# Optimization experiments

Hardware: AMD Instinct MI355X
Metric: run time of the kernel (lower is better)

The kernel has to match this reference:

```python
import jax, jax.numpy as jnp
import numpy as np

N_NODES = 50000
N_EDGES = 1600000
IN_DIM = 128
HID = 64
N_GRAPHS = 256


def gcn_conv(x, row, col, W, b, n_nodes):
    """PyG GCNConv: symmetric gcn_norm with self-loops, linear-then-aggregate."""
    h = x @ W  # [N, out]
    loop = jnp.arange(n_nodes, dtype=row.dtype)
    r = jnp.concatenate([row, loop])  # sources (messages from x[r])
    c = jnp.concatenate([col, loop])  # targets (aggregate at c)
    ew = jnp.ones(r.shape[0], dtype=x.dtype)
    deg = jax.ops.segment_sum(ew, c, num_segments=n_nodes)
    dinv = jnp.where(deg > 0, jax.lax.rsqrt(deg), 0.0).astype(x.dtype)
    norm = dinv[r] * dinv[c]  # [E+N]
    out = jax.ops.segment_sum(norm[:, None] * h[r], c, num_segments=n_nodes)
    return out + b


def global_mean_pool(x, batch, n_graphs):
    sums = jax.ops.segment_sum(x, batch, num_segments=n_graphs)
    cnt = jax.ops.segment_sum(jnp.ones(x.shape[0], x.dtype), batch, num_segments=n_graphs)
    return sums / jnp.clip(cnt, 1.0)[:, None]


def setup_inputs() -> dict:
    key = jax.random.key(0)
    ks = jax.random.split(key, 12)
    x = jax.random.normal(ks[0], (N_NODES, IN_DIM), dtype=jnp.float32)
    edge_index = jax.random.randint(ks[1], (2, N_EDGES), 0, N_NODES, dtype=jnp.int64)
    batch = jnp.sort(jax.random.randint(ks[2], (N_NODES,), 0, N_GRAPHS, dtype=jnp.int64))
    def glorot(k, shp):
        lim = float(np.sqrt(6.0 / (shp[0] + shp[1])))
        return jax.random.uniform(k, shp, jnp.float32, -lim, lim)
    return {
        "x": x,
        "edge_index": edge_index,
        "batch": batch,
        "W1": glorot(ks[3], (IN_DIM, HID)), "b1": jnp.zeros((HID,), jnp.float32),
        "W2": glorot(ks[4], (HID, HID)), "b2": jnp.zeros((HID,), jnp.float32),
        "W3": glorot(ks[5], (HID, HID)), "b3": jnp.zeros((HID,), jnp.float32),
        "Wl1": glorot(ks[6], (HID, 16)), "bl1": jnp.zeros((16,), jnp.float32),
        "Wl2": glorot(ks[7], (16, 1)), "bl2": jnp.zeros((1,), jnp.float32),
    }


def reference(x, edge_index, batch, W1, b1, W2, b2, W3, b3, Wl1, bl1, Wl2, bl2):
    n = x.shape[0]
    row, col = edge_index[0], edge_index[1]
    h = jax.nn.relu(gcn_conv(x, row, col, W1, b1, n))
    h = jax.nn.relu(gcn_conv(h, row, col, W2, b2, n))
    h = jax.nn.relu(gcn_conv(h, row, col, W3, b3, n))
    g = global_mean_pool(h, batch, N_GRAPHS)  # [G, 64]
    out = (g @ Wl1 + bl1) @ Wl2 + bl2  # [G, 1]
    return out
```

## Files before the change

kernel.cpp:

```cpp
#include <hip/hip_runtime.h>

#define HID 64
#define B1 512
#define NBMAX 200
#define CAP 10368
#define ENTCAP 3200
#define CPT 21

typedef __attribute__((ext_vector_type(8))) short short8;
typedef __attribute__((ext_vector_type(4))) float float4v;
typedef float f32x2 __attribute__((ext_vector_type(2)));

__device__ __forceinline__ ushort f2bf(float f) {
  unsigned u = __float_as_uint(f);
  unsigned r = (u + 0x7fffu + ((u >> 16) & 1u)) >> 16;
  return (ushort)r;
}
__device__ __forceinline__ float bf2f(ushort v) {
  return __uint_as_float(((unsigned)v) << 16);
}

__device__ __forceinline__ void acc8(f32x2& a01, f32x2& a23, uint2 d) {
  f32x2 t0, t1;
  t0.x = __uint_as_float(d.x << 16);
  t0.y = __uint_as_float(d.x & 0xffff0000u);
  t1.x = __uint_as_float(d.y << 16);
  t1.y = __uint_as_float(d.y & 0xffff0000u);
  a01 += t0;
  a23 += t1;
}


__global__ __launch_bounds__(256) void bucket_hist(const int* __restrict__ col, int E, int epb,
                                                   int* __restrict__ blockcnt,
                                                   const float* __restrict__ W1,
                                                   const float* __restrict__ W2,
                                                   const float* __restrict__ W3,
                                                   ushort* __restrict__ Wt1h, ushort* __restrict__ Wt1l,
                                                   ushort* __restrict__ Wt2h, ushort* __restrict__ Wt2l,
                                                   ushort* __restrict__ Wt3h, ushort* __restrict__ Wt3l) {
  int b = blockIdx.x, t = threadIdx.x;
  int gt = b * 256 + t;
  if (gt < 128 * 64) {
    int k = gt >> 6, nn = gt & 63;
    float w = W1[gt];
    ushort h = f2bf(w);
    Wt1h[nn * 128 + k] = h;
    Wt1l[nn * 128 + k] = f2bf(w - bf2f(h));
  }
  if (gt < 64 * 64) {
    int k = gt >> 6, nn = gt & 63;
    float w2 = W2[gt], w3 = W3[gt];
    ushort h2 = f2bf(w2), h3 = f2bf(w3);
    Wt2h[nn * 64 + k] = h2;
    Wt2l[nn * 64 + k] = f2bf(w2 - bf2f(h2));
    Wt3h[nn * 64 + k] = h3;
    Wt3l[nn * 64 + k] = f2bf(w3 - bf2f(h3));
  }

  __shared__ int cnt[256];
  cnt[t] = 0;
  __syncthreads();
  int lo = b * epb, hi = min(lo + epb, E);
  int ecnt = hi - lo;
  if (ecnt > 0) {
    int ecnt4 = ecnt & ~3;
    for (int i = t * 4; i < ecnt4; i += 1024) {
      int4 c4 = *(const int4*)&col[lo + i];
      atomicAdd(&cnt[c4.x >> 8], 1);
      atomicAdd(&cnt[c4.y >> 8], 1);
      atomicAdd(&cnt[c4.z >> 8], 1);
      atomicAdd(&cnt[c4.w >> 8], 1);
    }
    for (int i = ecnt4 + t; i < ecnt; i += 256) atomicAdd(&cnt[col[lo + i] >> 8], 1);
  }
  __syncthreads();
  blockcnt[b * 256 + t] = cnt[t];
}

__global__ __launch_bounds__(512) void scan_blocks(int* __restrict__ blockcnt,
                                                   int* __restrict__ buckettot) {
  __shared__ int s[512];
  int k = blockIdx.x;
  int t = threadIdx.x;
  int v = blockcnt[t * 256 + k];
  s[t] = v;
  __syncthreads();
  for (int d = 1; d < 512; d <<= 1) {
    int u = (t >= d) ? s[t - d] : 0;
    __syncthreads();
    s[t] += u;
    __syncthreads();
  }
  blockcnt[t * 256 + k] = s[t] - v;
  if (t == 511) buckettot[k] = s[t];
}

__global__ __launch_bounds__(256) void scan_buckettot(const int* __restrict__ buckettot,
                                                      int* __restrict__ bucketbase,
                                                      int* __restrict__ csr_off, int n, int E,
                                                      int nb) {
  __shared__ int s[256];
  int t = threadIdx.x;
  int v = buckettot[t];
  s[t] = v;
  __syncthreads();
  for (int d = 1; d < 256; d <<= 1) {
    int u = (t >= d) ? s[t - d] : 0;
    __syncthreads();
    s[t] += u;
    __syncthreads();
  }
  bucketbase[t] = s[t] - v;
  if (t == 255) bucketbase[256] = s[255];
  if (t == 0) csr_off[n] = E;
}

__global__ __launch_bounds__(256) void bin_edges(const int* __restrict__ row,
                                                 const int* __restrict__ col, int E, int epb,
                                                 const int* __restrict__ blockcnt,
                                                 const int* __restrict__ bucketbase,
                                                 unsigned* __restrict__ binned) {
  __shared__ int cnt[256];
  __shared__ int ofs[256];
  __shared__ int gb[256];
  __shared__ int lcur[256];
  __shared__ unsigned ent[ENTCAP];
  __shared__ unsigned stage[ENTCAP];
  int b = blockIdx.x, t = threadIdx.x;
  int lo = b * epb, hi = min(lo + epb, E);
  int ecnt = hi - lo;

  cnt[t] = 0;
  __syncthreads();
  if (ecnt > 0) {
    int ecnt4 = ecnt & ~3;
    for (int i = t * 4; i < ecnt4; i += 1024) {
      int4 c4 = *(const int4*)&col[lo + i];
      int4 r4 = *(const int4*)&row[lo + i];
      uint4 e4;
      e4.x = ((unsigned)r4.x << 16) | (unsigned)c4.x;
      e4.y = ((unsigned)r4.y << 16) | (unsigned)c4.y;
      e4.z = ((unsigned)r4.z << 16) | (unsigned)c4.z;
      e4.w = ((unsigned)r4.w << 16) | (unsigned)c4.w;
      *(uint4*)&ent[i] = e4;
      atomicAdd(&cnt[c4.x >> 8], 1);
      atomicAdd(&cnt[c4.y >> 8], 1);
      atomicAdd(&cnt[c4.z >> 8], 1);
      atomicAdd(&cnt[c4.w >> 8], 1);
    }
    for (int i = ecnt4 + t; i < ecnt; i += 256) {
      int c = col[lo + i];
      int r = row[lo + i];
      ent[i] = ((unsigned)r << 16) | (unsigned)c;
      atomicAdd(&cnt[c >> 8], 1);
    }
  }
  __syncthreads();
  int v = cnt[t];
  ofs[t] = v;
  __syncthreads();
  for (int d = 1; d < 256; d <<= 1) {
    int u = (t >= d) ? ofs[t - d] : 0;
    __syncthreads();
    ofs[t] += u;
    __syncthreads();
  }
  int excl = ofs[t] - v;
  int g = bucketbase[t] + blockcnt[b * 256 + t];
  __syncthreads();
  ofs[t] = excl;
  gb[t] = g;
  lcur[t] = excl;
  __syncthreads();
  if (ecnt > 0) {
    for (int i = t; i < ecnt; i += 256) {
      unsigned en = ent[i];
      int p = atomicAdd(&lcur[(en >> 8) & 255], 1);
      stage[p] = en;
    }
  }
  __syncthreads();
  if (ecnt > 0) {
    for (int i = t; i < ecnt; i += 256) {
      unsigned en = stage[i];
      int bb = (en >> 8) & 255;
      binned[gb[bb] + (i - ofs[bb])] = en;
    }
  }
}

__global__ __launch_bounds__(512) void bucket_csr(const unsigned* __restrict__ binned,
                                                  const int* __restrict__ bucketbase,
                                                  int* __restrict__ csr_off,
                                                  int* __restrict__ csr_src,
                                                  float* __restrict__ dinv, int n) {
  __shared__ int lcnt[256];
  __shared__ int lofs[256];
  __shared__ int lsrc[CAP];
  int k = blockIdx.x, t = threadIdx.x;
  int base = bucketbase[k], end = bucketbase[k + 1];
  int s = end - base;
  unsigned ent[CPT];
  if (t < 256) lcnt[t] = 0;
  __syncthreads();
#pragma unroll
  for (int q = 0; q < CPT; ++q) {
    int i = q * 512 + t;
    if (i < s) {
      unsigned p = binned[base + i];
      ent[q] = p;
      atomicAdd(&lcnt[p & 255u], 1);
    }
  }
  __syncthreads();
  int v = 0;
  if (t < 256) {
    v = lcnt[t];
    lofs[t] = v;
  }
  __syncthreads();
  for (int d = 1; d < 256; d <<= 1) {
    int u = (t < 256 && t >= d) ? lofs[t - d] : 0;
    __syncthreads();
    if (t < 256) lofs[t] += u;
    __syncthreads();
  }
  if (t < 256) {
    int excl = lofs[t] - v;
    int node = (k << 8) + t;
    if (node < n) {
      csr_off[node] = base + excl;
      dinv[node] = rsqrtf((float)(v + 1));
    }
    lcnt[t] = excl;
  }
  __syncthreads();
#pragma unroll
  for (int q = 0; q < CPT; ++q) {
    int i = q * 512 + t;
    if (i < s) {
      unsigned p = ent[q];
      int pos = atomicAdd(&lcnt[p & 255u], 1);
      if (pos < CAP) lsrc[pos] = (int)(p >> 16);
    }
  }
  __syncthreads();
  for (int i = t; i < s; i += 512) csr_src[base + i] = (i < CAP) ? lsrc[i] : 0;
}


template <int K>
__global__ __launch_bounds__(256) void gemm_mfma(const float* __restrict__ A,
                                                 const ushort* __restrict__ Wh,
                                                 const ushort* __restrict__ Wl,
                                                 const float* __restrict__ dinv,
                                                 ushort* __restrict__ out, int n) {
  int wave = (blockIdx.x * 256 + threadIdx.x) >> 6;
  int lane = threadIdx.x & 63;
  int row0 = wave * 16;
  if (row0 >= n) return;
  int m = lane & 15;
  int quad = lane >> 4;
  int r = row0 + m;
  int rc = (r < n) ? r : (n - 1);

  float4v acc[4];
#pragma unroll
  for (int t = 0; t < 4; ++t) acc[t] = (float4v){0.f, 0.f, 0.f, 0.f};

#pragma unroll
  for (int k0 = 0; k0 < K; k0 += 32) {
    const float4* xp = (const float4*)&A[(size_t)rc * K + k0 + quad * 8];
    float4 a0 = xp[0];
    float4 a1 = xp[1];
    float av[8] = {a0.x, a0.y, a0.z, a0.w, a1.x, a1.y, a1.z, a1.w};
    short8 ah, al;
#pragma unroll
    for (int i = 0; i < 8; ++i) {
      ushort h = f2bf(av[i]);
      ah[i] = (short)h;
      al[i] = (short)f2bf(av[i] - bf2f(h));
    }
#pragma unroll
    for (int t = 0; t < 4; ++t) {
      size_t wof = (size_t)(t * 16 + m) * K + k0 + quad * 8;
      short8 bh = *(const short8*)&Wh[wof];
      short8 bl = *(const short8*)&Wl[wof];
      acc[t] = __builtin_amdgcn_mfma_f32_16x16x32_bf16(ah, bh, acc[t], 0, 0, 0);
      acc[t] = __builtin_amdgcn_mfma_f32_16x16x32_bf16(al, bh, acc[t], 0, 0, 0);
      acc[t] = __builtin_amdgcn_mfma_f32_16x16x32_bf16(ah, bl, acc[t], 0, 0, 0);
    }
  }

  float4 dv = ((const float4*)dinv)[(row0 >> 2) + quad];
  float dvi[4] = {dv.x, dv.y, dv.z, dv.w};
#pragma unroll
  for (int i = 0; i < 4; ++i) {
    int orow = row0 + quad * 4 + i;
    if (orow < n) {
#pragma unroll
      for (int t = 0; t < 4; ++t) {
        out[(size_t)orow * 64 + t * 16 + m] = f2bf(dvi[i] * acc[t][i]);
      }
    }
  }
}


__global__ __launch_bounds__(256) void agg_kernel(
    const ushort* __restrict__ hs, const int* __restrict__ csr_off,
    const int* __restrict__ csr_src, const float* __restrict__ dinv,
    const float* __restrict__ bias, float* __restrict__ out, int n) {
  int wid = (blockIdx.x * 256 + threadIdx.x) >> 6;
  int lane = threadIdx.x & 63;
  if (wid >= n) return;
  int qe = lane >> 4;
  int fq = lane & 15;
  const uint2* hs2 = (const uint2*)hs;

  f32x2 a01 = {0.f, 0.f}, a23 = {0.f, 0.f};
  if (qe == 0) {
    acc8(a01, a23, hs2[(size_t)wid * 16 + fq]);
  }

  int j = csr_off[wid];
  int e = csr_off[wid + 1];

  int pre = min(e, (j + 3) & ~3);
  if (j + qe < pre) {
    int s0 = csr_src[j + qe];
    acc8(a01, a23, hs2[(size_t)s0 * 16 + fq]);
  }
  int base = pre;

  for (; base + 16 <= e; base += 16) {
    int4 s = *(const int4*)&csr_src[base + qe * 4];
    uint2 v0 = hs2[(size_t)s.x * 16 + fq];
    uint2 v1 = hs2[(size_t)s.y * 16 + fq];
    uint2 v2 = hs2[(size_t)s.z * 16 + fq];
    uint2 v3 = hs2[(size_t)s.w * 16 + fq];
    acc8(a01, a23, v0);
    acc8(a01, a23, v1);
    acc8(a01, a23, v2);
    acc8(a01, a23, v3);
  }

  for (; base + 4 <= e; base += 4) {
    int s0 = csr_src[base + qe];
    acc8(a01, a23, hs2[(size_t)s0 * 16 + fq]);
  }
  if (base + qe < e) {
    int s0 = csr_src[base + qe];
    acc8(a01, a23, hs2[(size_t)s0 * 16 + fq]);
  }

  a01.x += __shfl_xor(a01.x, 16, 64);
  a01.y += __shfl_xor(a01.y, 16, 64);
  a23.x += __shfl_xor(a23.x, 16, 64);
  a23.y += __shfl_xor(a23.y, 16, 64);
  a01.x += __shfl_xor(a01.x, 32, 64);
  a01.y += __shfl_xor(a01.y, 32, 64);
  a23.x += __shfl_xor(a23.x, 32, 64);
  a23.y += __shfl_xor(a23.y, 32, 64);

  if (qe == 0) {
    float d = dinv[wid];
    float4 bi = ((const float4*)bias)[fq];
    float4 r;
    r.x = fmaxf(d * a01.x + bi.x, 0.f);
    r.y = fmaxf(d * a01.y + bi.y, 0.f);
    r.z = fmaxf(d * a23.x + bi.z, 0.f);
    r.w = fmaxf(d * a23.y + bi.w, 0.f);
    ((float4*)out)[(size_t)wid * 16 + fq] = r;
  }
}


__global__ __launch_bounds__(256) void pool_mlp_kernel(
    const float* __restrict__ a, const int* __restrict__ batch, int n,
    const float* __restrict__ Wl1, const float* __restrict__ bl1,
    const float* __restrict__ Wl2, const float* __restrict__ bl2,
    float* __restrict__ out) {
  int g = blockIdx.x;
  int t = threadIdx.x;
  int lane = t & 63;
  int w = t >> 6;

  int lo = 0, hi = n;
  while (lo < hi) {
    int m = (lo + hi) >> 1;
    if (batch[m] < g) lo = m + 1; else hi = m;
  }
  int start = lo;
  lo = start; hi = n;
  while (lo < hi) {
    int m = (lo + hi) >> 1;
    if (batch[m] < g + 1) lo = m + 1; else hi = m;
  }
  int end = lo;

  float s = 0.f;
  for (int i = start + w; i < end; i += 4) s += a[i * 64 + lane];

  __shared__ float ps[4][64];
  __shared__ float gv[64];
  __shared__ float hv[16];
  ps[w][lane] = s;
  __syncthreads();
  if (w == 0) {
    float tot = ps[0][lane] + ps[1][lane] + ps[2][lane] + ps[3][lane];
    gv[lane] = tot / (float)max(end - start, 1);
  }
  __syncthreads();
  if (t < 16) {
    float h = bl1[t];
    for (int k = 0; k < 64; ++k) h += gv[k] * Wl1[k * 16 + t];
    hv[t] = h;
  }
  __syncthreads();
  if (t == 0) {
    float o = bl2[0];
    for (int j2 = 0; j2 < 16; ++j2) o += hv[j2] * Wl2[j2];
    out[g] = o;
  }
}


extern "C" void kernel_launch(void* const* d_in, const int* in_sizes, int n_in,
                              void* d_out, int out_size, void* d_ws, size_t ws_size,
                              hipStream_t stream) {
  const float* x = (const float*)d_in[0];
  const int* ei = (const int*)d_in[1];
  const int* batch = (const int*)d_in[2];
  const float* W1 = (const float*)d_in[3];
  const float* b1 = (const float*)d_in[4];
  const float* W2 = (const float*)d_in[5];
  const float* b2 = (const float*)d_in[6];
  const float* W3 = (const float*)d_in[7];
  const float* b3 = (const float*)d_in[8];
  const float* Wl1 = (const float*)d_in[9];
  const float* bl1 = (const float*)d_in[10];
  const float* Wl2 = (const float*)d_in[11];
  const float* bl2 = (const float*)d_in[12];

  int n = in_sizes[0] / 128;
  int E = in_sizes[1] / 2;
  int G = out_size;
  int nb = (n + 255) >> 8;
  int epb = (((E + B1 - 1) / B1) + 15) & ~15;

  const int* row = ei;
  const int* col = ei + E;

  char* p = (char*)d_ws;
  int* blockcnt = (int*)p;    p += B1 * 256 * 4;
  int* buckettot = (int*)p;   p += 256 * 4;
  int* bucketbase = (int*)p;  p += 272 * 4;
  int* csr_off = (int*)p;     p += 50064 * 4;
  float* dinv = (float*)p;    p += 50016 * 4;
  ushort* Wt1h = (ushort*)p;  p += 128 * 64 * 2;
  ushort* Wt1l = (ushort*)p;  p += 128 * 64 * 2;
  ushort* Wt2h = (ushort*)p;  p += 64 * 64 * 2;
  ushort* Wt2l = (ushort*)p;  p += 64 * 64 * 2;
  ushort* Wt3h = (ushort*)p;  p += 64 * 64 * 2;
  ushort* Wt3l = (ushort*)p;  p += 64 * 64 * 2;
  int* csr_src = (int*)p;     p += (size_t)((E + 15) / 16 * 16) * 4;
  ushort* hs = (ushort*)p;    p += (size_t)n * 64 * 2;
  float* abuf = (float*)p;
  unsigned* binned = (unsigned*)hs;

  bucket_hist<<<B1, 256, 0, stream>>>(col, E, epb, blockcnt,
                                      W1, W2, W3, Wt1h, Wt1l, Wt2h, Wt2l, Wt3h, Wt3l);
  scan_blocks<<<256, 512, 0, stream>>>(blockcnt, buckettot);
  scan_buckettot<<<1, 256, 0, stream>>>(buckettot, bucketbase, csr_off, n, E, nb);
  bin_edges<<<B1, 256, 0, stream>>>(row, col, E, epb, blockcnt, bucketbase, binned);
  bucket_csr<<<nb, 512, 0, stream>>>(binned, bucketbase, csr_off, csr_src, dinv, n);

  int nwaves = (n + 15) / 16;
  int gblocks = (nwaves + 3) / 4;
  int ablocks = (n * 64 + 255) / 256;

  gemm_mfma<128><<<gblocks, 256, 0, stream>>>(x, Wt1h, Wt1l, dinv, hs, n);
  agg_kernel<<<ablocks, 256, 0, stream>>>(hs, csr_off, csr_src, dinv, b1, abuf, n);
  gemm_mfma<64><<<gblocks, 256, 0, stream>>>(abuf, Wt2h, Wt2l, dinv, hs, n);
  agg_kernel<<<ablocks, 256, 0, stream>>>(hs, csr_off, csr_src, dinv, b2, abuf, n);
  gemm_mfma<64><<<gblocks, 256, 0, stream>>>(abuf, Wt3h, Wt3l, dinv, hs, n);
  agg_kernel<<<ablocks, 256, 0, stream>>>(hs, csr_off, csr_src, dinv, b3, abuf, n);
  pool_mlp_kernel<<<G, 256, 0, stream>>>(abuf, batch, n, Wl1, bl1, Wl2, bl2, (float*)d_out);
}
```

Baseline: 306.9 us.

## Fuse CSR build stages into one cooperative kernel with grid syncs

```diff
diff --git a/kernel.cpp b/kernel.cpp
--- a/kernel.cpp
+++ b/kernel.cpp
@@ -1,4 +1,7 @@
 #include <hip/hip_runtime.h>
+#include <hip/hip_cooperative_groups.h>
+
+namespace cg = cooperative_groups;
 
 #define HID 64
 #define B1 512
@@ -31,16 +34,26 @@
 }
 
 
-__global__ __launch_bounds__(256) void bucket_hist(const int* __restrict__ col, int E, int epb,
-                                                   int* __restrict__ blockcnt,
-                                                   const float* __restrict__ W1,
-                                                   const float* __restrict__ W2,
-                                                   const float* __restrict__ W3,
-                                                   ushort* __restrict__ Wt1h, ushort* __restrict__ Wt1l,
-                                                   ushort* __restrict__ Wt2h, ushort* __restrict__ Wt2l,
-                                                   ushort* __restrict__ Wt3h, ushort* __restrict__ Wt3l) {
+__global__ __launch_bounds__(256) void build_fused(
+    const int* __restrict__ row, const int* __restrict__ col, int E, int epb, int n,
+    int* __restrict__ blockcnt, int* __restrict__ buckettot,
+    int* __restrict__ bucketbase, int* __restrict__ csr_off,
+    unsigned* __restrict__ binned,
+    const float* __restrict__ W1, const float* __restrict__ W2, const float* __restrict__ W3,
+    ushort* __restrict__ Wt1h, ushort* __restrict__ Wt1l,
+    ushort* __restrict__ Wt2h, ushort* __restrict__ Wt2l,
+    ushort* __restrict__ Wt3h, ushort* __restrict__ Wt3l) {
+  __shared__ int cnt[256];
+  __shared__ int ofs[256];
+  __shared__ int gb[256];
+  __shared__ int lcur[256];
+  __shared__ int s[256];
+  __shared__ unsigned ent[ENTCAP];
+  __shared__ unsigned stage[ENTCAP];
+  cg::grid_group grid = cg::this_grid();
   int b = blockIdx.x, t = threadIdx.x;
   int gt = b * 256 + t;
+
   if (gt < 128 * 64) {
     int k = gt >> 6, nn = gt & 63;
     float w = W1[gt];
@@ -58,76 +71,6 @@
     Wt3l[nn * 64 + k] = f2bf(w3 - bf2f(h3));
   }
 
-  __shared__ int cnt[256];
-  cnt[t] = 0;
-  __syncthreads();
-  int lo = b * epb, hi = min(lo + epb, E);
-  int ecnt = hi - lo;
-  if (ecnt > 0) {
-    int ecnt4 = ecnt & ~3;
-    for (int i = t * 4; i < ecnt4; i += 1024) {
-      int4 c4 = *(const int4*)&col[lo + i];
-      atomicAdd(&cnt[c4.x >> 8], 1);
-      atomicAdd(&cnt[c4.y >> 8], 1);
-      atomicAdd(&cnt[c4.z >> 8], 1);
-      atomicAdd(&cnt[c4.w >> 8], 1);
-    }
-    for (int i = ecnt4 + t; i < ecnt; i += 256) atomicAdd(&cnt[col[lo + i] >> 8], 1);
-  }
-  __syncthreads();
-  blockcnt[b * 256 + t] = cnt[t];
-}
-
-__global__ __launch_bounds__(512) void scan_blocks(int* __restrict__ blockcnt,
-                                                   int* __restrict__ buckettot) {
-  __shared__ int s[512];
-  int k = blockIdx.x;
-  int t = threadIdx.x;
-  int v = blockcnt[t * 256 + k];
-  s[t] = v;
-  __syncthreads();
-  for (int d = 1; d < 512; d <<= 1) {
-    int u = (t >= d) ? s[t - d] : 0;
-    __syncthreads();
-    s[t] += u;
-    __syncthreads();
-  }
-  blockcnt[t * 256 + k] = s[t] - v;
-  if (t == 511) buckettot[k] = s[t];
-}
-
-__global__ __launch_bounds__(256) void scan_buckettot(const int* __restrict__ buckettot,
-                                                      int* __restrict__ bucketbase,
-                                                      int* __restrict__ csr_off, int n, int E,
-                                                      int nb) {
-  __shared__ int s[256];
-  int t = threadIdx.x;
-  int v = buckettot[t];
-  s[t] = v;
-  __syncthreads();
-  for (int d = 1; d < 256; d <<= 1) {
-    int u = (t >= d) ? s[t - d] : 0;
-    __syncthreads();
-    s[t] += u;
-    __syncthreads();
-  }
-  bucketbase[t] = s[t] - v;
-  if (t == 255) bucketbase[256] = s[255];
-  if (t == 0) csr_off[n] = E;
-}
-
-__global__ __launch_bounds__(256) void bin_edges(const int* __restrict__ row,
-                                                 const int* __restrict__ col, int E, int epb,
-                                                 const int* __restrict__ blockcnt,
-                                                 const int* __restrict__ bucketbase,
-                                                 unsigned* __restrict__ binned) {
-  __shared__ int cnt[256];
-  __shared__ int ofs[256];
-  __shared__ int gb[256];
-  __shared__ int lcur[256];
-  __shared__ unsigned ent[ENTCAP];
-  __shared__ unsigned stage[ENTCAP];
-  int b = blockIdx.x, t = threadIdx.x;
   int lo = b * epb, hi = min(lo + epb, E);
   int ecnt = hi - lo;
 
@@ -157,6 +100,44 @@
     }
   }
   __syncthreads();
+  blockcnt[b * 256 + t] = cnt[t];
+  if (gt == 0) csr_off[n] = E;
+  grid.sync();
+
+  if (b < 256) {
+    int a0 = blockcnt[(2 * t) * 256 + b];
+    int a1 = blockcnt[(2 * t + 1) * 256 + b];
+    int pair = a0 + a1;
+    s[t] = pair;
+    __syncthreads();
+    for (int d = 1; d < 256; d <<= 1) {
+      int u = (t >= d) ? s[t - d] : 0;
+      __syncthreads();
+      s[t] += u;
+      __syncthreads();
+    }
+    int inc = s[t];
+    int excl = inc - pair;
+    blockcnt[(2 * t) * 256 + b] = excl;
+    blockcnt[(2 * t + 1) * 256 + b] = excl + a0;
+    if (t == 255) buckettot[b] = inc;
+  }
+  grid.sync();
+
+  int bt = buckettot[t];
+  s[t] = bt;
+  __syncthreads();
+  for (int d = 1; d < 256; d <<= 1) {
+    int u = (t >= d) ? s[t - d] : 0;
+    __syncthreads();
+    s[t] += u;
+    __syncthreads();
+  }
+  int bb = s[t] - bt;
+  if (b == 0) {
+    bucketbase[t] = bb;
+    if (t == 255) bucketbase[256] = s[255];
+  }
   int v = cnt[t];
   ofs[t] = v;
   __syncthreads();
@@ -167,7 +148,7 @@
     __syncthreads();
   }
   int excl = ofs[t] - v;
-  int g = bucketbase[t] + blockcnt[b * 256 + t];
+  int g = bb + blockcnt[b * 256 + t];
   __syncthreads();
   ofs[t] = excl;
   gb[t] = g;
@@ -184,8 +165,8 @@
   if (ecnt > 0) {
     for (int i = t; i < ecnt; i += 256) {
       unsigned en = stage[i];
-      int bb = (en >> 8) & 255;
-      binned[gb[bb] + (i - ofs[bb])] = en;
+      int bbk = (en >> 8) & 255;
+      binned[gb[bbk] + (i - ofs[bbk])] = en;
     }
   }
 }
@@ -334,12 +315,33 @@
   }
   int base = pre;
 
+  for (; base + 32 <= e; base += 32) {
+    int4 s0 = *(const int4*)&csr_src[base + qe * 4];
+    int4 s1 = *(const int4*)&csr_src[base + 16 + qe * 4];
+    uint2 v0 = hs2[(size_t)s0.x * 16 + fq];
+    uint2 v1 = hs2[(size_t)s0.y * 16 + fq];
+    uint2 v2 = hs2[(size_t)s0.z * 16 + fq];
+    uint2 v3 = hs2[(size_t)s0.w * 16 + fq];
+    uint2 v4 = hs2[(size_t)s1.x * 16 + fq];
+    uint2 v5 = hs2[(size_t)s1.y * 16 + fq];
+    uint2 v6 = hs2[(size_t)s1.z * 16 + fq];
+    uint2 v7 = hs2[(size_t)s1.w * 16 + fq];
+    acc8(a01, a23, v0);
+    acc8(a01, a23, v1);
+    acc8(a01, a23, v2);
+    acc8(a01, a23, v3);
+    acc8(a01, a23, v4);
+    acc8(a01, a23, v5);
+    acc8(a01, a23, v6);
+    acc8(a01, a23, v7);
+  }
+
   for (; base + 16 <= e; base += 16) {
-    int4 s = *(const int4*)&csr_src[base + qe * 4];
-    uint2 v0 = hs2[(size_t)s.x * 16 + fq];
-    uint2 v1 = hs2[(size_t)s.y * 16 + fq];
-    uint2 v2 = hs2[(size_t)s.z * 16 + fq];
-    uint2 v3 = hs2[(size_t)s.w * 16 + fq];
+    int4 s0 = *(const int4*)&csr_src[base + qe * 4];
+    uint2 v0 = hs2[(size_t)s0.x * 16 + fq];
+    uint2 v1 = hs2[(size_t)s0.y * 16 + fq];
+    uint2 v2 = hs2[(size_t)s0.z * 16 + fq];
+    uint2 v3 = hs2[(size_t)s0.w * 16 + fq];
     acc8(a01, a23, v0);
     acc8(a01, a23, v1);
     acc8(a01, a23, v2);
@@ -470,11 +472,12 @@
   float* abuf = (float*)p;
   unsigned* binned = (unsigned*)hs;
 
-  bucket_hist<<<B1, 256, 0, stream>>>(col, E, epb, blockcnt,
-                                      W1, W2, W3, Wt1h, Wt1l, Wt2h, Wt2l, Wt3h, Wt3l);
-  scan_blocks<<<256, 512, 0, stream>>>(blockcnt, buckettot);
-  scan_buckettot<<<1, 256, 0, stream>>>(buckettot, bucketbase, csr_off, n, E, nb);
-  bin_edges<<<B1, 256, 0, stream>>>(row, col, E, epb, blockcnt, bucketbase, binned);
+  void* bargs[] = {(void*)&row, (void*)&col, (void*)&E, (void*)&epb, (void*)&n,
+                   (void*)&blockcnt, (void*)&buckettot, (void*)&bucketbase, (void*)&csr_off,
+                   (void*)&binned, (void*)&W1, (void*)&W2, (void*)&W3,
+                   (void*)&Wt1h, (void*)&Wt1l, (void*)&Wt2h, (void*)&Wt2l,
+                   (void*)&Wt3h, (void*)&Wt3l};
+  hipLaunchCooperativeKernel((const void*)build_fused, dim3(B1), dim3(256), bargs, 0, stream);
   bucket_csr<<<nb, 512, 0, stream>>>(binned, bucketbase, csr_off, csr_src, dinv, n);
 
   int nwaves = (n + 15) / 16;
```

Measured after the change: 432.0 us. 40.8% more time.

## Split edge aggregation into two feature-half passes

Applied to the files above, without the earlier changes.

```diff
diff --git a/kernel.cpp b/kernel.cpp
--- a/kernel.cpp
+++ b/kernel.cpp
@@ -308,53 +308,67 @@
 }
 
 
-__global__ __launch_bounds__(256) void agg_kernel(
+template <int FH>
+__global__ __launch_bounds__(256) void agg_half(
     const ushort* __restrict__ hs, const int* __restrict__ csr_off,
     const int* __restrict__ csr_src, const float* __restrict__ dinv,
     const float* __restrict__ bias, float* __restrict__ out, int n) {
   int wid = (blockIdx.x * 256 + threadIdx.x) >> 6;
   int lane = threadIdx.x & 63;
   if (wid >= n) return;
-  int qe = lane >> 4;
-  int fq = lane & 15;
+  int qe = lane >> 3;
+  int fl = lane & 7;
   const uint2* hs2 = (const uint2*)hs;
+  const int fb = FH * 8 + fl;
 
   f32x2 a01 = {0.f, 0.f}, a23 = {0.f, 0.f};
   if (qe == 0) {
-    acc8(a01, a23, hs2[(size_t)wid * 16 + fq]);
+    acc8(a01, a23, hs2[(size_t)wid * 16 + fb]);
   }
 
   int j = csr_off[wid];
   int e = csr_off[wid + 1];
 
-  int pre = min(e, (j + 3) & ~3);
+  int pre = min(e, (j + 7) & ~7);
   if (j + qe < pre) {
     int s0 = csr_src[j + qe];
-    acc8(a01, a23, hs2[(size_t)s0 * 16 + fq]);
+    acc8(a01, a23, hs2[(size_t)s0 * 16 + fb]);
   }
   int base = pre;
 
-  for (; base + 16 <= e; base += 16) {
+  for (; base + 32 <= e; base += 32) {
     int4 s = *(const int4*)&csr_src[base + qe * 4];
-    uint2 v0 = hs2[(size_t)s.x * 16 + fq];
-    uint2 v1 = hs2[(size_t)s.y * 16 + fq];
-    uint2 v2 = hs2[(size_t)s.z * 16 + fq];
-    uint2 v3 = hs2[(size_t)s.w * 16 + fq];
+    uint2 v0 = hs2[(size_t)s.x * 16 + fb];
+    uint2 v1 = hs2[(size_t)s.y * 16 + fb];
+    uint2 v2 = hs2[(size_t)s.z * 16 + fb];
+    uint2 v3 = hs2[(size_t)s.w * 16 + fb];
     acc8(a01, a23, v0);
     acc8(a01, a23, v1);
     acc8(a01, a23, v2);
     acc8(a01, a23, v3);
   }
 
-  for (; base + 4 <= e; base += 4) {
+  for (; base + 16 <= e; base += 16) {
+    int2 s = *(const int2*)&csr_src[base + qe * 2];
+    uint2 v0 = hs2[(size_t)s.x * 16 + fb];
+    uint2 v1 = hs2[(size_t)s.y * 16 + fb];
+    acc8(a01, a23, v0);
+    acc8(a01, a23, v1);
+  }
+
+  for (; base + 8 <= e; base += 8) {
     int s0 = csr_src[base + qe];
-    acc8(a01, a23, hs2[(size_t)s0 * 16 + fq]);
+    acc8(a01, a23, hs2[(size_t)s0 * 16 + fb]);
   }
   if (base + qe < e) {
     int s0 = csr_src[base + qe];
-    acc8(a01, a23, hs2[(size_t)s0 * 16 + fq]);
-  }
-
+    acc8(a01, a23, hs2[(size_t)s0 * 16 + fb]);
+  }
+
+  a01.x += __shfl_xor(a01.x, 8, 64);
+  a01.y += __shfl_xor(a01.y, 8, 64);
+  a23.x += __shfl_xor(a23.x, 8, 64);
+  a23.y += __shfl_xor(a23.y, 8, 64);
   a01.x += __shfl_xor(a01.x, 16, 64);
   a01.y += __shfl_xor(a01.y, 16, 64);
   a23.x += __shfl_xor(a23.x, 16, 64);
@@ -366,13 +380,13 @@
 
   if (qe == 0) {
     float d = dinv[wid];
-    float4 bi = ((const float4*)bias)[fq];
+    float4 bi = ((const float4*)bias)[fb];
     float4 r;
     r.x = fmaxf(d * a01.x + bi.x, 0.f);
     r.y = fmaxf(d * a01.y + bi.y, 0.f);
     r.z = fmaxf(d * a23.x + bi.z, 0.f);
     r.w = fmaxf(d * a23.y + bi.w, 0.f);
-    ((float4*)out)[(size_t)wid * 16 + fq] = r;
+    ((float4*)out)[(size_t)wid * 16 + fb] = r;
   }
 }
 
@@ -482,10 +496,13 @@
   int ablocks = (n * 64 + 255) / 256;
 
   gemm_mfma<128><<<gblocks, 256, 0, stream>>>(x, Wt1h, Wt1l, dinv, hs, n);
-  agg_kernel<<<ablocks, 256, 0, stream>>>(hs, csr_off, csr_src, dinv, b1, abuf, n);
+  agg_half<0><<<ablocks, 256, 0, stream>>>(hs, csr_off, csr_src, dinv, b1, abuf, n);
+  agg_half<1><<<ablocks, 256, 0, stream>>>(hs, csr_off, csr_src, dinv, b1, abuf, n);
   gemm_mfma<64><<<gblocks, 256, 0, stream>>>(abuf, Wt2h, Wt2l, dinv, hs, n);
-  agg_kernel<<<ablocks, 256, 0, stream>>>(hs, csr_off, csr_src, dinv, b2, abuf, n);
+  agg_half<0><<<ablocks, 256, 0, stream>>>(hs, csr_off, csr_src, dinv, b2, abuf, n);
+  agg_half<1><<<ablocks, 256, 0, stream>>>(hs, csr_off, csr_src, dinv, b2, abuf, n);
   gemm_mfma<64><<<gblocks, 256, 0, stream>>>(abuf, Wt3h, Wt3l, dinv, hs, n);
-  agg_kernel<<<ablocks, 256, 0, stream>>>(hs, csr_off, csr_src, dinv, b3, abuf, n);
+  agg_half<0><<<ablocks, 256, 0, stream>>>(hs, csr_off, csr_src, dinv, b3, abuf, n);
+  agg_half<1><<<ablocks, 256, 0, stream>>>(hs, csr_off, csr_src, dinv, b3, abuf, n);
   pool_mlp_kernel<<<G, 256, 0, stream>>>(abuf, batch, n, Wl1, bl1, Wl2, bl2, (float*)d_out);
 }
```

Result: slower. 375.8 us (+22.4%).
